# Kernel tuning notes

Measured on AMD Instinct MI355X. Metric: run time of the kernel, lower is better.

Reference implementation:

```python
import jax, jax.numpy as jnp
import numpy as np

N_NODES = 50000
N_EDGES = 600000
EMB_DIM = 128
HIDDEN = 128
BN_EPS = 1e-5


def setup_inputs() -> dict:
    key = jax.random.key(0)
    ks = jax.random.split(key, 8)
    s_in = 1.0 / np.sqrt(EMB_DIM)
    s_h = 1.0 / np.sqrt(HIDDEN)
    return {
        "x_idx": jnp.arange(N_NODES, dtype=jnp.int32),
        "edge_index": jax.random.randint(ks[0], (2, N_EDGES), 0, N_NODES, dtype=jnp.int32),
        "emb_table": jax.random.normal(ks[1], (N_NODES, EMB_DIM), jnp.float32),
        # ClusterGCNConv: lin_out (bias=False) and lin_root (bias=False)
        "W_out": jax.random.uniform(ks[2], (HIDDEN, EMB_DIM), jnp.float32, -s_in, s_in),
        "W_root": jax.random.uniform(ks[3], (HIDDEN, EMB_DIM), jnp.float32, -s_in, s_in),
        "bn0_gamma": jnp.ones((HIDDEN,), jnp.float32),
        "bn0_beta": jnp.zeros((HIDDEN,), jnp.float32),
        # SGConv 1 (K=1, add_self_loops=True, Linear with bias)
        "W_sg1": jax.random.uniform(ks[4], (HIDDEN, HIDDEN), jnp.float32, -s_h, s_h),
        "b_sg1": jnp.zeros((HIDDEN,), jnp.float32),
        "bn1_gamma": jnp.ones((HIDDEN,), jnp.float32),
        "bn1_beta": jnp.zeros((HIDDEN,), jnp.float32),
        # SGConv 2 (final layer)
        "W_sg2": jax.random.uniform(ks[5], (HIDDEN, HIDDEN), jnp.float32, -s_h, s_h),
        "b_sg2": jnp.zeros((HIDDEN,), jnp.float32),
    }


def _cluster_gcn(x, row, col, W_out, W_root, n):
    # PyG ClusterGCNConv (add_self_loops=False, diag_lambda=0, bias=False):
    # out[c] = sum_{(r->c)} (1/deg(c)) * x[r];  return out @ W_out^T + x @ W_root^T
    deg = jax.ops.segment_sum(jnp.ones_like(col, dtype=x.dtype), col, num_segments=n)
    deg_inv = 1.0 / jnp.maximum(deg, 1.0)
    msg = x[row] * deg_inv[col][:, None]                  # [E, D]
    agg = jax.ops.segment_sum(msg, col, num_segments=n)   # [N, D]
    return agg @ W_out.T + x @ W_root.T


def _sg_conv(x, row, col, W, b, n):
    # PyG SGConv K=1 with gcn_norm: A_hat = D^{-1/2}(A+I)D^{-1/2}, then Linear.
    loop = jnp.arange(n, dtype=row.dtype)
    r = jnp.concatenate([row, loop])
    c = jnp.concatenate([col, loop])
    deg = jax.ops.segment_sum(jnp.ones_like(c, dtype=x.dtype), c, num_segments=n)
    dis = jnp.where(deg > 0, jax.lax.rsqrt(jnp.maximum(deg, 1e-12)), 0.0)
    ew = dis[r] * dis[c]                                   # [E+N]
    agg = jax.ops.segment_sum(x[r] * ew[:, None], c, num_segments=n)
    return agg @ W.T + b


def _bn(x, gamma, beta):
    # BatchNorm1d in training mode: batch statistics, biased variance.
    mu = x.mean(axis=0)
    var = ((x - mu) ** 2).mean(axis=0)
    return (x - mu) * jax.lax.rsqrt(var + BN_EPS) * gamma + beta


def reference(x_idx, edge_index, emb_table, W_out, W_root, bn0_gamma, bn0_beta,
              W_sg1, b_sg1, bn1_gamma, bn1_beta, W_sg2, b_sg2):
    n = emb_table.shape[0]
    row, col = edge_index[0], edge_index[1]
    x = emb_table[x_idx]                                   # [N, D]
    # layer 0: ClusterGCNConv -> BN -> ReLU (dropout p=0)
    x = _cluster_gcn(x, row, col, W_out, W_root, n)
    x = jax.nn.relu(_bn(x, bn0_gamma, bn0_beta))
    # layer 1: SGConv -> BN -> ReLU
    x = _sg_conv(x, row, col, W_sg1, b_sg1, n)
    x = jax.nn.relu(_bn(x, bn1_gamma, bn1_beta))
    # final SGConv
    return _sg_conv(x, row, col, W_sg2, b_sg2, n)
```

## Files before the change

kernel.cpp:

```cpp
#include <hip/hip_runtime.h>
#include <stdint.h>

#define NN 50000
#define NE 600000
#define DD 128
#define BN_EPS 1e-5f

typedef __attribute__((ext_vector_type(8))) short short8;
typedef __attribute__((ext_vector_type(4))) float f32x4;

__device__ __forceinline__ float bf2f(uint16_t u) {
    union { uint32_t u; float f; } v; v.u = ((uint32_t)u) << 16; return v.f;
}
__device__ __forceinline__ uint16_t f2bf(float f) {
    union { float f; uint32_t u; } v; v.f = f;
    return (uint16_t)((v.u + 0x7FFFu + ((v.u >> 16) & 1u)) >> 16);
}
__device__ __forceinline__ float lo16(uint32_t v) { return bf2f((uint16_t)(v & 0xFFFFu)); }
__device__ __forceinline__ float hi16(uint32_t v) { return bf2f((uint16_t)(v >> 16)); }

__global__ void k_zero(uint4* __restrict__ p, int n16) {
    int i = blockIdx.x * 256 + threadIdx.x;
    if (i < n16) p[i] = make_uint4(0u, 0u, 0u, 0u);
}

__global__ void k_count(const int* __restrict__ col, int* __restrict__ cnt) {
    int e = blockIdx.x * 256 + threadIdx.x;
    if (e < NE) atomicAdd(&cnt[col[e]], 1);
}

__global__ void k_alloc(const int* __restrict__ cnt, int* __restrict__ cursor,
                        int* __restrict__ off, int* __restrict__ fillp,
                        float* __restrict__ deginv, float* __restrict__ dis) {
    int i = blockIdx.x * 256 + threadIdx.x;
    int lane = threadIdx.x & 63;
    int deg = (i < NN) ? cnt[i] : 0;
    int v = deg;
    #pragma unroll
    for (int d = 1; d < 64; d <<= 1) {
        int t = __shfl_up(v, d, 64);
        if (lane >= d) v += t;
    }
    int total = __shfl(v, 63, 64);
    int wbase = 0;
    if (lane == 63) wbase = atomicAdd(cursor, total);
    wbase = __shfl(wbase, 63, 64);
    int base = wbase + v - deg;
    if (i < NN) {
        off[i] = base;
        fillp[i] = base;
        deginv[i] = 1.0f / fmaxf((float)deg, 1.0f);
        dis[i] = rsqrtf((float)deg + 1.0f);
    }
}

__global__ void k_fill(const int* __restrict__ ei, int* __restrict__ fillp,
                       int* __restrict__ csr_row) {
    int e = blockIdx.x * 256 + threadIdx.x;
    if (e < NE) {
        int c = ei[NE + e];
        int p = atomicAdd(&fillp[c], 1);
        csr_row[p] = ei[e];
    }
}

__global__ void k_gather(const int* __restrict__ x_idx, const float* __restrict__ emb,
                         uint16_t* __restrict__ xb) {
    int idx = blockIdx.x * 256 + threadIdx.x;
    if (idx >= NN * 32) return;
    int node = idx >> 5, c4 = (idx & 31) << 2;
    int src = x_idx[node];
    float4 v = *(const float4*)(emb + (size_t)src * DD + c4);
    ushort4 o;
    o.x = f2bf(v.x); o.y = f2bf(v.y); o.z = f2bf(v.z); o.w = f2bf(v.w);
    *(ushort4*)(xb + (size_t)node * DD + c4) = o;
}

template<int MODE>
__global__ __launch_bounds__(256)
void k_agg(const uint16_t* __restrict__ xb, const int* __restrict__ off,
           const int* __restrict__ cnt, const int* __restrict__ csr_row,
           const float* __restrict__ deginv, const float* __restrict__ dis,
           uint16_t* __restrict__ aggb) {
    int node = blockIdx.x * 4 + (threadIdx.x >> 6);
    if (node >= NN) return;
    int lane = threadIdx.x & 63;
    const uint32_t* __restrict__ xw = (const uint32_t*)xb;
    float a0 = 0.0f, a1 = 0.0f;
    if (MODE == 1) {
        uint32_t v = xw[(size_t)node * 64 + lane];
        a0 = lo16(v); a1 = hi16(v);
    }
    int s = off[node], e = s + cnt[node];
    for (int base = s; base < e; base += 64) {
        int c64 = min(e - base, 64);
        int idxv = (lane < c64) ? csr_row[base + lane] : 0;
        int i = 0;
        for (; i + 8 <= c64; i += 8) {
            uint32_t v[8];
            #pragma unroll
            for (int u = 0; u < 8; ++u) {
                int r = __builtin_amdgcn_readlane(idxv, i + u);
                v[u] = xw[(size_t)r * 64 + lane];
            }
            #pragma unroll
            for (int u = 0; u < 8; ++u) { a0 += lo16(v[u]); a1 += hi16(v[u]); }
        }
        if (i + 4 <= c64) {
            uint32_t v[4];
            #pragma unroll
            for (int u = 0; u < 4; ++u) {
                int r = __builtin_amdgcn_readlane(idxv, i + u);
                v[u] = xw[(size_t)r * 64 + lane];
            }
            #pragma unroll
            for (int u = 0; u < 4; ++u) { a0 += lo16(v[u]); a1 += hi16(v[u]); }
            i += 4;
        }
        for (; i < c64; ++i) {
            int r = __builtin_amdgcn_readlane(idxv, i);
            uint32_t v = xw[(size_t)r * 64 + lane];
            a0 += lo16(v); a1 += hi16(v);
        }
    }
    float sc = (MODE == 1) ? dis[node] : deginv[node];
    a0 *= sc; a1 *= sc;
    uint32_t o = (uint32_t)f2bf(a0) | ((uint32_t)f2bf(a1) << 16);
    *(uint32_t*)(aggb + (size_t)node * DD + lane * 2) = o;
}

template<bool DUAL, bool STATS, bool BIAS, bool STORE_BF16>
__global__ __launch_bounds__(256, 2)
void k_gemm(const uint16_t* __restrict__ A1, const uint16_t* __restrict__ A2,
            const float* __restrict__ W1, const float* __restrict__ W2,
            const float* __restrict__ bias, float* __restrict__ Hf,
            uint16_t* __restrict__ Hb, float* __restrict__ stats) {
    __shared__ uint16_t Alds[128 * 128];
    __shared__ uint16_t Wlds[128 * 128];
    const int t = threadIdx.x;
    const int lane = t & 63, wid = t >> 6;
    const int wm = (wid >> 1) * 64, wn = (wid & 1) * 64;
    const int m0 = blockIdx.x * 128;
    f32x4 zero = {0.0f, 0.0f, 0.0f, 0.0f};
    f32x4 acc[4][4];
    #pragma unroll
    for (int m = 0; m < 4; ++m)
        #pragma unroll
        for (int n = 0; n < 4; ++n) acc[m][n] = zero;

    const int NP = DUAL ? 2 : 1;
    for (int p = 0; p < NP; ++p) {
        const uint16_t* A = (DUAL && p) ? A2 : A1;
        const float* W = (DUAL && p) ? W2 : W1;
        if (p) __syncthreads();
        #pragma unroll
        for (int it = 0; it < 8; ++it) {
            int idx = it * 256 + t;
            int row = idx >> 4, c16 = idx & 15;
            uint32_t boff = (uint32_t)(row * 256 + ((c16 * 16) ^ ((row & 7) << 4)));
            uint4 v = make_uint4(0u, 0u, 0u, 0u);
            if (m0 + row < NN)
                v = *(const uint4*)(A + (size_t)(m0 + row) * DD + c16 * 8);
            *(uint4*)((char*)Alds + boff) = v;
        }
        #pragma unroll
        for (int it = 0; it < 8; ++it) {
            int idx = it * 256 + t;
            int row = idx >> 4, c8 = idx & 15;
            const float* wp = W + row * DD + c8 * 8;
            float4 v0 = *(const float4*)(wp);
            float4 v1 = *(const float4*)(wp + 4);
            uint4 pk;
            pk.x = (uint32_t)f2bf(v0.x) | ((uint32_t)f2bf(v0.y) << 16);
            pk.y = (uint32_t)f2bf(v0.z) | ((uint32_t)f2bf(v0.w) << 16);
            pk.z = (uint32_t)f2bf(v1.x) | ((uint32_t)f2bf(v1.y) << 16);
            pk.w = (uint32_t)f2bf(v1.z) | ((uint32_t)f2bf(v1.w) << 16);
            uint32_t boff = (uint32_t)(row * 256 + ((c8 * 16) ^ ((row & 7) << 4)));
            *(uint4*)((char*)Wlds + boff) = pk;
        }
        __syncthreads();
        #pragma unroll
        for (int ks = 0; ks < 4; ++ks) {
            short8 a[4], b[4];
            int kb = ks * 64 + ((lane >> 4) << 4);
            #pragma unroll
            for (int m = 0; m < 4; ++m) {
                int row = wm + m * 16 + (lane & 15);
                a[m] = *(const short8*)((const char*)Alds + row * 256 + (kb ^ ((row & 7) << 4)));
            }
            #pragma unroll
            for (int n = 0; n < 4; ++n) {
                int row = wn + n * 16 + (lane & 15);
                b[n] = *(const short8*)((const char*)Wlds + row * 256 + (kb ^ ((row & 7) << 4)));
            }
            #pragma unroll
            for (int m = 0; m < 4; ++m)
                #pragma unroll
                for (int n = 0; n < 4; ++n)
                    acc[m][n] = __builtin_amdgcn_mfma_f32_16x16x32_bf16(a[m], b[n], acc[m][n], 0, 0, 0);
        }
    }
    #pragma unroll
    for (int n = 0; n < 4; ++n) {
        int col = wn + n * 16 + (lane & 15);
        float bb = BIAS ? bias[col] : 0.0f;
        float ssum = 0.0f, ssq = 0.0f;
        #pragma unroll
        for (int m = 0; m < 4; ++m) {
            int rbase = m0 + wm + m * 16 + ((lane >> 4) << 2);
            #pragma unroll
            for (int i = 0; i < 4; ++i) {
                int gr = rbase + i;
                if (gr < NN) {
                    float v = acc[m][n][i] + bb;
                    if (STORE_BF16) Hb[(size_t)gr * DD + col] = f2bf(v);
                    else            Hf[(size_t)gr * DD + col] = v;
                    ssum += v; ssq += v * v;
                }
            }
        }
        if (STATS) {
            ssum += __shfl_xor(ssum, 16, 64);
            ssum += __shfl_xor(ssum, 32, 64);
            ssq  += __shfl_xor(ssq, 16, 64);
            ssq  += __shfl_xor(ssq, 32, 64);
            if (lane < 16) {
                atomicAdd(&stats[col], ssum);
                atomicAdd(&stats[DD + col], ssq);
            }
        }
    }
}

__global__ __launch_bounds__(256)
void k_bnrelu(const uint16_t* __restrict__ Hb, const float* __restrict__ st,
              const float* __restrict__ gamma, const float* __restrict__ beta,
              const float* __restrict__ dis, uint16_t* __restrict__ xb) {
    __shared__ float s_sc[128], s_of[128];
    int t = threadIdx.x;
    if (t < 128) {
        const float invn = 1.0f / (float)NN;
        float mean = st[t] * invn;
        float var = st[DD + t] * invn - mean * mean;
        float sc = gamma[t] * rsqrtf(var + BN_EPS);
        s_sc[t] = sc;
        s_of[t] = beta[t] - mean * sc;
    }
    __syncthreads();
    int idx = blockIdx.x * 256 + t;
    int node = idx >> 4, c8 = (idx & 15) << 3;
    if (node >= NN) return;
    float d = dis[node];
    uint4 h = *(const uint4*)(Hb + (size_t)node * DD + c8);
    uint32_t hw[4] = {h.x, h.y, h.z, h.w};
    uint32_t ow[4];
    #pragma unroll
    for (int j = 0; j < 4; ++j) {
        int c = c8 + j * 2;
        float v0 = fmaxf(lo16(hw[j]) * s_sc[c]     + s_of[c],     0.0f) * d;
        float v1 = fmaxf(hi16(hw[j]) * s_sc[c + 1] + s_of[c + 1], 0.0f) * d;
        ow[j] = (uint32_t)f2bf(v0) | ((uint32_t)f2bf(v1) << 16);
    }
    uint4 o = make_uint4(ow[0], ow[1], ow[2], ow[3]);
    *(uint4*)(xb + (size_t)node * DD + c8) = o;
}

extern "C" void kernel_launch(void* const* d_in, const int* in_sizes, int n_in,
                              void* d_out, int out_size, void* d_ws, size_t ws_size,
                              hipStream_t stream) {
    const int* x_idx   = (const int*)d_in[0];
    const int* ei      = (const int*)d_in[1];
    const float* emb   = (const float*)d_in[2];
    const float* W_out = (const float*)d_in[3];
    const float* W_root= (const float*)d_in[4];
    const float* g0    = (const float*)d_in[5];
    const float* be0   = (const float*)d_in[6];
    const float* W1    = (const float*)d_in[7];
    const float* b1    = (const float*)d_in[8];
    const float* g1    = (const float*)d_in[9];
    const float* be1   = (const float*)d_in[10];
    const float* W2    = (const float*)d_in[11];
    const float* b2    = (const float*)d_in[12];
    float* out = (float*)d_out;

    char* ws = (char*)d_ws;
    size_t o = 0;
    auto carve = [&](size_t bytes) -> void* {
        void* p = ws + o;
        o = (o + bytes + 255) & ~(size_t)255;
        return p;
    };
    int* cnt      = (int*)carve((size_t)NN * 4);
    int* cursor   = (int*)carve(4);
    float* st0    = (float*)carve(256 * 4);
    float* st1    = (float*)carve(256 * 4);
    size_t zlen = o;
    int* fillp    = (int*)carve((size_t)NN * 4);
    int* off      = (int*)carve((size_t)NN * 4);
    float* deginv = (float*)carve((size_t)NN * 4);
    float* dis    = (float*)carve((size_t)NN * 4);
    int* csr_row  = (int*)carve((size_t)NE * 4);
    uint16_t* xb  = (uint16_t*)carve((size_t)NN * DD * 2);
    uint16_t* aggb= (uint16_t*)carve((size_t)NN * DD * 2);
    uint16_t* hb  = (uint16_t*)carve((size_t)NN * DD * 2);

    const int ZB = (int)((zlen / 16 + 255) / 256);
    const int EB = (NE + 255) / 256;
    const int NB = (NN + 255) / 256;
    const int GB = (NN + 127) / 128;
    const int AB = (NN + 3) / 4;
    const int VB = (NN * 32 + 255) / 256;
    const int BB = (NN * 16 + 255) / 256;

    k_zero<<<ZB, 256, 0, stream>>>((uint4*)ws, (int)(zlen / 16));
    k_count<<<EB, 256, 0, stream>>>(ei + NE, cnt);
    k_alloc<<<NB, 256, 0, stream>>>(cnt, cursor, off, fillp, deginv, dis);
    k_fill<<<EB, 256, 0, stream>>>(ei, fillp, csr_row);
    k_gather<<<VB, 256, 0, stream>>>(x_idx, emb, xb);

    k_agg<0><<<AB, 256, 0, stream>>>(xb, off, cnt, csr_row, deginv, dis, aggb);
    k_gemm<true, true, false, true><<<GB, 256, 0, stream>>>(
        aggb, xb, W_out, W_root, nullptr, nullptr, hb, st0);
    k_bnrelu<<<BB, 256, 0, stream>>>(hb, st0, g0, be0, dis, xb);

    k_agg<1><<<AB, 256, 0, stream>>>(xb, off, cnt, csr_row, deginv, dis, aggb);
    k_gemm<false, true, true, true><<<GB, 256, 0, stream>>>(
        aggb, nullptr, W1, nullptr, b1, nullptr, hb, st1);
    k_bnrelu<<<BB, 256, 0, stream>>>(hb, st1, g1, be1, dis, xb);

    k_agg<1><<<AB, 256, 0, stream>>>(xb, off, cnt, csr_row, deginv, dis, aggb);
    k_gemm<false, false, true, false><<<GB, 256, 0, stream>>>(
        aggb, nullptr, W2, nullptr, b2, out, nullptr, nullptr);
}
```

Baseline: 268.7 us.

## Fuse BN+ReLU into neighbor aggregation and merge count with embedding gather

Removes the separate BatchNorm/ReLU kernels by applying the per-channel affine, ReLU and source-degree scaling on the fly inside the gather-aggregation, reading the raw GEMM output directly. The aggregation now uses two waves per node, one per 64-channel half, with 16-bit loads per lane, and fetches the neighbor dis values via readlane. Edge counting and the embedding gather are merged into one launch. This saves two full read/write passes over the node features and a few launches, at the cost of redoing the BN/ReLU math per edge and using narrower per-lane loads in the gather.

```diff
diff --git a/kernel.cpp b/kernel.cpp
--- a/kernel.cpp
+++ b/kernel.cpp
@@ -24,9 +24,24 @@
     if (i < n16) p[i] = make_uint4(0u, 0u, 0u, 0u);
 }
 
-__global__ void k_count(const int* __restrict__ col, int* __restrict__ cnt) {
-    int e = blockIdx.x * 256 + threadIdx.x;
-    if (e < NE) atomicAdd(&cnt[col[e]], 1);
+#define EB ((NE + 255) / 256)
+__global__ void k_pre(const int* __restrict__ ei, int* __restrict__ cnt,
+                      const int* __restrict__ x_idx, const float* __restrict__ emb,
+                      uint16_t* __restrict__ xb) {
+    int b = blockIdx.x;
+    if (b < EB) {
+        int e = b * 256 + threadIdx.x;
+        if (e < NE) atomicAdd(&cnt[ei[NE + e]], 1);
+    } else {
+        int idx = (b - EB) * 256 + threadIdx.x;
+        if (idx >= NN * 32) return;
+        int node = idx >> 5, c4 = (idx & 31) << 2;
+        int src = x_idx[node];
+        float4 v = *(const float4*)(emb + (size_t)src * DD + c4);
+        ushort4 o;
+        o.x = f2bf(v.x); o.y = f2bf(v.y); o.z = f2bf(v.z); o.w = f2bf(v.w);
+        *(ushort4*)(xb + (size_t)node * DD + c4) = o;
+    }
 }
 
 __global__ void k_alloc(const int* __restrict__ cnt, int* __restrict__ cursor,
@@ -64,69 +79,81 @@
     }
 }
 
-__global__ void k_gather(const int* __restrict__ x_idx, const float* __restrict__ emb,
-                         uint16_t* __restrict__ xb) {
-    int idx = blockIdx.x * 256 + threadIdx.x;
-    if (idx >= NN * 32) return;
-    int node = idx >> 5, c4 = (idx & 31) << 2;
-    int src = x_idx[node];
-    float4 v = *(const float4*)(emb + (size_t)src * DD + c4);
-    ushort4 o;
-    o.x = f2bf(v.x); o.y = f2bf(v.y); o.z = f2bf(v.z); o.w = f2bf(v.w);
-    *(ushort4*)(xb + (size_t)node * DD + c4) = o;
-}
-
 template<int MODE>
 __global__ __launch_bounds__(256)
-void k_agg(const uint16_t* __restrict__ xb, const int* __restrict__ off,
+void k_agg(const uint16_t* __restrict__ X, const int* __restrict__ off,
            const int* __restrict__ cnt, const int* __restrict__ csr_row,
            const float* __restrict__ deginv, const float* __restrict__ dis,
-           uint16_t* __restrict__ aggb) {
-    int node = blockIdx.x * 4 + (threadIdx.x >> 6);
+           const float* __restrict__ st, const float* __restrict__ gamma,
+           const float* __restrict__ beta, uint16_t* __restrict__ aggb) {
+    int gw = blockIdx.x * 4 + (threadIdx.x >> 6);
+    int node = gw >> 1, h = gw & 1;
     if (node >= NN) return;
     int lane = threadIdx.x & 63;
-    const uint32_t* __restrict__ xw = (const uint32_t*)xb;
-    float a0 = 0.0f, a1 = 0.0f;
+    int c = h * 64 + lane;
+    float sc = 0.0f, of = 0.0f;
     if (MODE == 1) {
-        uint32_t v = xw[(size_t)node * 64 + lane];
-        a0 = lo16(v); a1 = hi16(v);
+        const float invn = 1.0f / (float)NN;
+        float mean = st[c] * invn;
+        float var = st[DD + c] * invn - mean * mean;
+        sc = gamma[c] * rsqrtf(var + BN_EPS);
+        of = beta[c] - mean * sc;
+    }
+    float a = 0.0f;
+    if (MODE == 1) {
+        float hv = bf2f(X[(size_t)node * DD + c]);
+        a = fmaxf(hv * sc + of, 0.0f) * dis[node];
     }
     int s = off[node], e = s + cnt[node];
     for (int base = s; base < e; base += 64) {
         int c64 = min(e - base, 64);
         int idxv = (lane < c64) ? csr_row[base + lane] : 0;
+        int disb = 0;
+        if (MODE == 1) {
+            float dv = (lane < c64) ? dis[idxv] : 0.0f;
+            disb = __float_as_int(dv);
+        }
         int i = 0;
         for (; i + 8 <= c64; i += 8) {
-            uint32_t v[8];
+            uint16_t v[8]; float w[8];
             #pragma unroll
             for (int u = 0; u < 8; ++u) {
                 int r = __builtin_amdgcn_readlane(idxv, i + u);
-                v[u] = xw[(size_t)r * 64 + lane];
-            }
-            #pragma unroll
-            for (int u = 0; u < 8; ++u) { a0 += lo16(v[u]); a1 += hi16(v[u]); }
+                if (MODE == 1) w[u] = __int_as_float(__builtin_amdgcn_readlane(disb, i + u));
+                v[u] = X[(size_t)r * DD + c];
+            }
+            #pragma unroll
+            for (int u = 0; u < 8; ++u) {
+                if (MODE == 1) a += w[u] * fmaxf(bf2f(v[u]) * sc + of, 0.0f);
+                else           a += bf2f(v[u]);
+            }
         }
         if (i + 4 <= c64) {
-            uint32_t v[4];
+            uint16_t v[4]; float w[4];
             #pragma unroll
             for (int u = 0; u < 4; ++u) {
                 int r = __builtin_amdgcn_readlane(idxv, i + u);
-                v[u] = xw[(size_t)r * 64 + lane];
-            }
-            #pragma unroll
-            for (int u = 0; u < 4; ++u) { a0 += lo16(v[u]); a1 += hi16(v[u]); }
+                if (MODE == 1) w[u] = __int_as_float(__builtin_amdgcn_readlane(disb, i + u));
+                v[u] = X[(size_t)r * DD + c];
+            }
+            #pragma unroll
+            for (int u = 0; u < 4; ++u) {
+                if (MODE == 1) a += w[u] * fmaxf(bf2f(v[u]) * sc + of, 0.0f);
+                else           a += bf2f(v[u]);
+            }
             i += 4;
         }
         for (; i < c64; ++i) {
             int r = __builtin_amdgcn_readlane(idxv, i);
-            uint32_t v = xw[(size_t)r * 64 + lane];
-            a0 += lo16(v); a1 += hi16(v);
-        }
-    }
-    float sc = (MODE == 1) ? dis[node] : deginv[node];
-    a0 *= sc; a1 *= sc;
-    uint32_t o = (uint32_t)f2bf(a0) | ((uint32_t)f2bf(a1) << 16);
-    *(uint32_t*)(aggb + (size_t)node * DD + lane * 2) = o;
+            uint16_t v = X[(size_t)r * DD + c];
+            if (MODE == 1) {
+                float w = __int_as_float(__builtin_amdgcn_readlane(disb, i));
+                a += w * fmaxf(bf2f(v) * sc + of, 0.0f);
+            } else a += bf2f(v);
+        }
+    }
+    a *= (MODE == 1) ? dis[node] : deginv[node];
+    aggb[(size_t)node * DD + c] = f2bf(a);
 }
 
 template<bool DUAL, bool STATS, bool BIAS, bool STORE_BF16>
@@ -230,39 +257,6 @@
             }
         }
     }
-}
-
-__global__ __launch_bounds__(256)
-void k_bnrelu(const uint16_t* __restrict__ Hb, const float* __restrict__ st,
-              const float* __restrict__ gamma, const float* __restrict__ beta,
-              const float* __restrict__ dis, uint16_t* __restrict__ xb) {
-    __shared__ float s_sc[128], s_of[128];
-    int t = threadIdx.x;
-    if (t < 128) {
-        const float invn = 1.0f / (float)NN;
-        float mean = st[t] * invn;
-        float var = st[DD + t] * invn - mean * mean;
-        float sc = gamma[t] * rsqrtf(var + BN_EPS);
-        s_sc[t] = sc;
-        s_of[t] = beta[t] - mean * sc;
-    }
-    __syncthreads();
-    int idx = blockIdx.x * 256 + t;
-    int node = idx >> 4, c8 = (idx & 15) << 3;
-    if (node >= NN) return;
-    float d = dis[node];
-    uint4 h = *(const uint4*)(Hb + (size_t)node * DD + c8);
-    uint32_t hw[4] = {h.x, h.y, h.z, h.w};
-    uint32_t ow[4];
-    #pragma unroll
-    for (int j = 0; j < 4; ++j) {
-        int c = c8 + j * 2;
-        float v0 = fmaxf(lo16(hw[j]) * s_sc[c]     + s_of[c],     0.0f) * d;
-        float v1 = fmaxf(hi16(hw[j]) * s_sc[c + 1] + s_of[c + 1], 0.0f) * d;
-        ow[j] = (uint32_t)f2bf(v0) | ((uint32_t)f2bf(v1) << 16);
-    }
-    uint4 o = make_uint4(ow[0], ow[1], ow[2], ow[3]);
-    *(uint4*)(xb + (size_t)node * DD + c8) = o;
 }
 
 extern "C" void kernel_launch(void* const* d_in, const int* in_sizes, int n_in,
@@ -305,30 +299,28 @@
     uint16_t* hb  = (uint16_t*)carve((size_t)NN * DD * 2);
 
     const int ZB = (int)((zlen / 16 + 255) / 256);
-    const int EB = (NE + 255) / 256;
     const int NB = (NN + 255) / 256;
     const int GB = (NN + 127) / 128;
-    const int AB = (NN + 3) / 4;
+    const int AB = (NN * 2 + 3) / 4;
     const int VB = (NN * 32 + 255) / 256;
-    const int BB = (NN * 16 + 255) / 256;
 
     k_zero<<<ZB, 256, 0, stream>>>((uint4*)ws, (int)(zlen / 16));
-    k_count<<<EB, 256, 0, stream>>>(ei + NE, cnt);
+    k_pre<<<EB + VB, 256, 0, stream>>>(ei, cnt, x_idx, emb, xb);
     k_alloc<<<NB, 256, 0, stream>>>(cnt, cursor, off, fillp, deginv, dis);
     k_fill<<<EB, 256, 0, stream>>>(ei, fillp, csr_row);
-    k_gather<<<VB, 256, 0, stream>>>(x_idx, emb, xb);
-
-    k_agg<0><<<AB, 256, 0, stream>>>(xb, off, cnt, csr_row, deginv, dis, aggb);
+
+    k_agg<0><<<AB, 256, 0, stream>>>(xb, off, cnt, csr_row, deginv, dis,
+                                     nullptr, nullptr, nullptr, aggb);
     k_gemm<true, true, false, true><<<GB, 256, 0, stream>>>(
         aggb, xb, W_out, W_root, nullptr, nullptr, hb, st0);
-    k_bnrelu<<<BB, 256, 0, stream>>>(hb, st0, g0, be0, dis, xb);
-
-    k_agg<1><<<AB, 256, 0, stream>>>(xb, off, cnt, csr_row, deginv, dis, aggb);
+
+    k_agg<1><<<AB, 256, 0, stream>>>(hb, off, cnt, csr_row, deginv, dis,
+                                     st0, g0, be0, aggb);
     k_gemm<false, true, true, true><<<GB, 256, 0, stream>>>(
         aggb, nullptr, W1, nullptr, b1, nullptr, hb, st1);
-    k_bnrelu<<<BB, 256, 0, stream>>>(hb, st1, g1, be1, dis, xb);
-
-    k_agg<1><<<AB, 256, 0, stream>>>(xb, off, cnt, csr_row, deginv, dis, aggb);
+
+    k_agg<1><<<AB, 256, 0, stream>>>(hb, off, cnt, csr_row, deginv, dis,
+                                     st1, g1, be1, aggb);
     k_gemm<false, false, true, false><<<GB, 256, 0, stream>>>(
         aggb, nullptr, W2, nullptr, b2, out, nullptr, nullptr);
 }
```

After: 304.9 us. 1.13x slower.
